# Kernel tuning notes

Measured on AMD Instinct MI355X. Metric: run time of the kernel, lower is better.

## Reference

```python
import jax, jax.numpy as jnp
import numpy as np

N, E, G, D, H, C = 50000, 800000, 64, 128, 4, 32
EPS = 1e-5  # GraphNorm eps


def _gcn(x, W, b, src, dst, n):
    # PyG GCNConv: add self-loops (done by caller), symmetric norm D^-1/2 A D^-1/2
    xw = x @ W
    deg = jax.ops.segment_sum(jnp.ones_like(dst, dtype=xw.dtype), dst, num_segments=n)
    dinv = jnp.where(deg > 0, jax.lax.rsqrt(jnp.maximum(deg, 1e-12)), 0.0)
    norm = dinv[src] * dinv[dst]                      # [E2]
    out = jax.ops.segment_sum(xw[src] * norm[:, None], dst, num_segments=n)
    return out + b


def _gat(x, W, a_src, a_dst, b, src, dst, n):
    # PyG GATConv, heads=H, out C per head, concat, leaky_relu slope 0.2, self-loops added by caller
    h = (x @ W).reshape(n, H, C)
    es = jnp.einsum('nhc,hc->nh', h, a_src)
    ed = jnp.einsum('nhc,hc->nh', h, a_dst)
    e = jax.nn.leaky_relu(es[src] + ed[dst], 0.2)     # [E2,H]
    m = jax.ops.segment_max(e, dst, num_segments=n)   # per-dst softmax (stable)
    e = jnp.exp(e - m[dst])
    s = jax.ops.segment_sum(e, dst, num_segments=n)
    alpha = e / (s[dst] + 1e-16)
    out = jax.ops.segment_sum(h[src] * alpha[:, :, None], dst, num_segments=n)
    return out.reshape(n, H * C) + b


def _graphnorm(x, batch, w, b, ms, g):
    cnt = jnp.maximum(jax.ops.segment_sum(jnp.ones((x.shape[0],), x.dtype), batch, num_segments=g), 1.0)
    mean = jax.ops.segment_sum(x, batch, num_segments=g) / cnt[:, None]
    sub = x - ms * mean[batch]
    var = jax.ops.segment_sum(sub * sub, batch, num_segments=g) / cnt[:, None]
    return w * sub * jax.lax.rsqrt(var[batch] + EPS) + b


def setup_inputs() -> dict:
    key = jax.random.key(0)
    ks = jax.random.split(key, 40)

    def lin(k, din, dout):
        return jax.random.normal(k, (din, dout), jnp.float32) * np.float32((2.0 / (din + dout)) ** 0.5)

    inp = {
        'x': jax.random.normal(ks[0], (N, D), jnp.float32),
        'edge_index': jax.random.randint(ks[1], (2, E), 0, N, dtype=jnp.int32),
        'batch': jnp.sort(jax.random.randint(ks[2], (N,), 0, G, dtype=jnp.int32)),
        'Wp': lin(ks[3], D, D), 'bp': jnp.zeros((D,), jnp.float32),
        'Wg': lin(ks[4], D, D), 'bg': jnp.zeros((D,), jnp.float32),
        'Wa1': lin(ks[5], D, H * C), 'as1': jax.random.normal(ks[6], (H, C), jnp.float32) * 0.1,
        'ad1': jax.random.normal(ks[7], (H, C), jnp.float32) * 0.1, 'ba1': jnp.zeros((D,), jnp.float32),
        'Wa2': lin(ks[8], D, H * C), 'as2': jax.random.normal(ks[9], (H, C), jnp.float32) * 0.1,
        'ad2': jax.random.normal(ks[10], (H, C), jnp.float32) * 0.1, 'ba2': jnp.zeros((D,), jnp.float32),
        'gnw0': jnp.ones((D,), jnp.float32), 'gnb0': jnp.zeros((D,), jnp.float32), 'gns0': jnp.ones((D,), jnp.float32),
        'gnw1': jnp.ones((D,), jnp.float32), 'gnb1': jnp.zeros((D,), jnp.float32), 'gns1': jnp.ones((D,), jnp.float32),
        'gnw2': jnp.ones((D,), jnp.float32), 'gnb2': jnp.zeros((D,), jnp.float32), 'gns2': jnp.ones((D,), jnp.float32),
        'hw1': lin(ks[11], 2 * D, D), 'hb1': jnp.zeros((D,), jnp.float32),
        'hw2': lin(ks[12], D, D // 2), 'hb2': jnp.zeros((D // 2,), jnp.float32),
        'hw3': lin(ks[13], D // 2, 2), 'hb3': jnp.zeros((2,), jnp.float32),
        'nw1': lin(ks[14], D, D // 2), 'nb1': jnp.zeros((D // 2,), jnp.float32),
        'nw2': lin(ks[15], D // 2, 1), 'nb2': jnp.zeros((1,), jnp.float32),
    }
    return inp


def reference(x, edge_index, batch, Wp, bp, Wg, bg, Wa1, as1, ad1, ba1, Wa2, as2, ad2, ba2,
              gnw0, gnb0, gns0, gnw1, gnb1, gns1, gnw2, gnb2, gns2,
              hw1, hb1, hw2, hb2, hw3, hb3, nw1, nb1, nw2, nb2):
    n = x.shape[0]
    loop = jnp.arange(n, dtype=edge_index.dtype)
    src = jnp.concatenate([edge_index[0], loop])
    dst = jnp.concatenate([edge_index[1], loop])

    x = x @ Wp + bp
    h = _graphnorm(_gcn(x, Wg, bg, src, dst, n), batch, gnw0, gnb0, gns0, G)
    x = jax.nn.relu(h) + x  # dropout is identity in eval mode
    h = _graphnorm(_gat(x, Wa1, as1, ad1, ba1, src, dst, n), batch, gnw1, gnb1, gns1, G)
    x = jax.nn.relu(h) + x
    h = _graphnorm(_gat(x, Wa2, as2, ad2, ba2, src, dst, n), batch, gnw2, gnb2, gns2, G)
    x = jax.nn.relu(h) + x

    node_hub_scores = jax.nn.sigmoid((jax.nn.relu(x @ nw1 + nb1) @ nw2 + nb2)[:, 0])

    cnt = jnp.maximum(jax.ops.segment_sum(jnp.ones((n,), x.dtype), batch, num_segments=G), 1.0)
    gmean = jax.ops.segment_sum(x, batch, num_segments=G) / cnt[:, None]
    gmax = jax.ops.segment_max(x, batch, num_segments=G)
    graph_features = jnp.concatenate([gmean, gmax], axis=1)  # [G, 2D]

    z = jax.nn.relu(graph_features @ hw1 + hb1)
    z = jax.nn.relu(z @ hw2 + hb2)
    logits = z @ hw3 + hb3
    return (logits, node_hub_scores, graph_features, x)
```

## Files before the change

### kernel.cpp

```cpp
#include <hip/hip_runtime.h>
#include <cstdint>

#define D 128
#define GG 64
#define SLICES 16
#define NXCD 8

typedef short bf16x8 __attribute__((ext_vector_type(8)));
typedef float f32x4 __attribute__((ext_vector_type(4)));

__device__ inline unsigned short bf16u(float f) {
  unsigned u = __float_as_uint(f);
  u = (u + 0x7FFFu + ((u >> 16) & 1u)) >> 16;
  return (unsigned short)u;
}
__device__ inline float2 unpackbf2(unsigned u) {
  return make_float2(__uint_as_float(u << 16), __uint_as_float(u & 0xFFFF0000u));
}
__device__ inline void accum8(float* acc, uint4 v, float w) {
  float2 p0 = unpackbf2(v.x), p1 = unpackbf2(v.y), p2 = unpackbf2(v.z), p3 = unpackbf2(v.w);
  acc[0] += p0.x * w; acc[1] += p0.y * w; acc[2] += p1.x * w; acc[3] += p1.y * w;
  acc[4] += p2.x * w; acc[5] += p2.y * w; acc[6] += p3.x * w; acc[7] += p3.y * w;
}

__global__ void count_edges_k(const int* __restrict__ dst, int* __restrict__ cnt, int E) {
  int e = blockIdx.x * blockDim.x + threadIdx.x;
  if (e < E) atomicAdd(&cnt[dst[e]], 1);
}

__global__ void bounds_init_k(int* __restrict__ gstart, int* __restrict__ gend) {
  int g = threadIdx.x;
  gstart[g] = 0;
  gend[g] = 0;
}

__global__ void graph_bounds_k(const int* __restrict__ batch, int* __restrict__ gstart,
                               int* __restrict__ gend, int n) {
  int i = blockIdx.x * blockDim.x + threadIdx.x;
  if (i >= n) return;
  int b = batch[i];
  if (i == 0) {
    gstart[b] = 0;
  } else {
    int pb = batch[i - 1];
    if (pb != b) { gstart[b] = i; gend[pb] = i; }
  }
  if (i == n - 1) gend[b] = n;
}

__global__ void gcnt_k(const int* __restrict__ gstart, const int* __restrict__ gend,
                       int* __restrict__ gcnt) {
  int g = threadIdx.x;
  gcnt[g] = gend[g] - gstart[g];
}

__global__ __launch_bounds__(256) void scan1_k(const int* __restrict__ cnt, int* __restrict__ rp,
                                               int* __restrict__ bsum, int n) {
  __shared__ int sd[256];
  int t = threadIdx.x;
  int i = blockIdx.x * 256 + t;
  int v = (i < n) ? cnt[i] : 0;
  sd[t] = v;
  __syncthreads();
#pragma unroll
  for (int off = 1; off < 256; off <<= 1) {
    int u = (t >= off) ? sd[t - off] : 0;
    __syncthreads();
    sd[t] += u;
    __syncthreads();
  }
  if (i < n) rp[i] = sd[t] - v;
  if (t == 255) bsum[blockIdx.x] = sd[255];
}

__global__ __launch_bounds__(256) void scan2_k(int* __restrict__ bsum, int nb) {
  __shared__ int sd[256];
  int t = threadIdx.x;
  int v = (t < nb) ? bsum[t] : 0;
  sd[t] = v;
  __syncthreads();
#pragma unroll
  for (int off = 1; off < 256; off <<= 1) {
    int u = (t >= off) ? sd[t - off] : 0;
    __syncthreads();
    sd[t] += u;
    __syncthreads();
  }
  if (t < nb) bsum[t] = sd[t] - v;
}

__global__ __launch_bounds__(256) void scan3_k(int* __restrict__ rp, const int* __restrict__ bsum,
                                               int* __restrict__ cur, const int* __restrict__ cnt,
                                               float* __restrict__ dinv, int n, int E) {
  int i = blockIdx.x * 256 + threadIdx.x;
  if (i < n) {
    int r = rp[i] + bsum[blockIdx.x];
    rp[i] = r;
    cur[i] = r;
    dinv[i] = rsqrtf((float)cnt[i] + 1.0f);
  }
  if (i == 0) rp[n] = E;
}

__global__ __launch_bounds__(256) void fill_csr_xcd_k(const int* __restrict__ src,
                                                      const int* __restrict__ dst,
                                                      int* __restrict__ cur,
                                                      unsigned short* __restrict__ col,
                                                      int E, int slice) {
  int pass = blockIdx.x & (NXCD - 1);
  int e = (blockIdx.x >> 3) * 256 + threadIdx.x;
  if (e >= E) return;
  int d = dst[e];
  if ((unsigned)(d - pass * slice) < (unsigned)slice) {
    int p = atomicAdd(&cur[d], 1);
    col[p] = (unsigned short)src[e];
  }
}

__global__ void cast_bf16_k(const float* __restrict__ in, unsigned short* __restrict__ outp, int n4) {
  int i = blockIdx.x * blockDim.x + threadIdx.x;
  if (i >= n4) return;
  float4 v = ((const float4*)in)[i];
  ushort4 o;
  o.x = bf16u(v.x); o.y = bf16u(v.y); o.z = bf16u(v.z); o.w = bf16u(v.w);
  ((ushort4*)outp)[i] = o;
}

__global__ void packB_k(const float* __restrict__ B, unsigned short* __restrict__ Bp, int ldb, int ct) {
  int idx = blockIdx.x * 256 + threadIdx.x;
  if (idx >= ct * 256) return;
  int lane = idx & 63;
  int kc = (idx >> 6) & 3;
  int c = idx >> 8;
  int kb = kc * 32 + (lane >> 4) * 8;
  int colq = c * 16 + (lane & 15);
  unsigned short o[8];
#pragma unroll
  for (int j = 0; j < 8; ++j) o[j] = bf16u(B[(size_t)(kb + j) * ldb + colq]);
  uint4 p;
  p.x = (unsigned)o[0] | ((unsigned)o[1] << 16);
  p.y = (unsigned)o[2] | ((unsigned)o[3] << 16);
  p.z = (unsigned)o[4] | ((unsigned)o[5] << 16);
  p.w = (unsigned)o[6] | ((unsigned)o[7] << 16);
  *(uint4*)&Bp[(size_t)idx * 8] = p;
}

__global__ __launch_bounds__(256) void gemm_mfma_k(const unsigned short* __restrict__ Ab,
                                                   const unsigned short* __restrict__ Bp,
                                                   const float* __restrict__ bias,
                                                   float* __restrict__ Cf,
                                                   unsigned short* __restrict__ Cb,
                                                   const float* __restrict__ rowscale,
                                                   const float* __restrict__ as_flat,
                                                   const float* __restrict__ ad_flat,
                                                   float* __restrict__ es, float* __restrict__ ed,
                                                   int M) {
  __shared__ unsigned short Bs[16384];
  int t = threadIdx.x;
  for (int i = t; i < 2048; i += 256) ((uint4*)Bs)[i] = ((const uint4*)Bp)[i];
  __syncthreads();
  int w = t >> 6, lane = t & 63;
  int row0 = blockIdx.x * 64 + w * 16;
  int arow = row0 + (lane & 15);
  f32x4 acc[8];
#pragma unroll
  for (int c = 0; c < 8; ++c) acc[c] = {0.f, 0.f, 0.f, 0.f};
#pragma unroll
  for (int kc = 0; kc < 4; ++kc) {
    bf16x8 a = {0, 0, 0, 0, 0, 0, 0, 0};
    if (arow < M) a = *(const bf16x8*)&Ab[(size_t)arow * 128 + kc * 32 + (lane >> 4) * 8];
#pragma unroll
    for (int c = 0; c < 8; ++c) {
      bf16x8 b = *(const bf16x8*)&Bs[((c * 4 + kc) * 64 + lane) * 8];
      acc[c] = __builtin_amdgcn_mfma_f32_16x16x32_bf16(a, b, acc[c], 0, 0, 0);
    }
  }
  int l15 = lane & 15;
  int rbase = row0 + (lane >> 4) * 4;
#pragma unroll
  for (int c = 0; c < 8; ++c) {
    int colq = c * 16 + l15;
    float bb = bias ? bias[colq] : 0.f;
#pragma unroll
    for (int r = 0; r < 4; ++r) {
      int row = rbase + r;
      if (row < M) {
        float v = acc[c][r] + bb;
        if (Cf) Cf[(size_t)row * 128 + colq] = v;
        if (Cb) {
          float rs = rowscale ? rowscale[row] : 1.f;
          Cb[(size_t)row * 128 + colq] = bf16u(v * rs);
        }
      }
    }
  }
  if (as_flat) {
    float pe[4][4], pd[4][4];
#pragma unroll
    for (int h = 0; h < 4; ++h) {
      float a0 = as_flat[h * 32 + l15], a1 = as_flat[h * 32 + 16 + l15];
      float d0 = ad_flat[h * 32 + l15], d1 = ad_flat[h * 32 + 16 + l15];
#pragma unroll
      for (int r = 0; r < 4; ++r) {
        pe[h][r] = acc[2 * h][r] * a0 + acc[2 * h + 1][r] * a1;
        pd[h][r] = acc[2 * h][r] * d0 + acc[2 * h + 1][r] * d1;
      }
    }
#pragma unroll
    for (int off = 1; off < 16; off <<= 1) {
#pragma unroll
      for (int h = 0; h < 4; ++h)
#pragma unroll
        for (int r = 0; r < 4; ++r) {
          pe[h][r] += __shfl_xor(pe[h][r], off, 64);
          pd[h][r] += __shfl_xor(pd[h][r], off, 64);
        }
    }
    int hh = l15 & 3, rr = l15 >> 2;
    int row = rbase + rr;
    if (row < M) {
      es[row * 4 + hh] = pe[hh][rr];
      ed[row * 4 + hh] = pd[hh][rr];
    }
  }
}

__global__ __launch_bounds__(256) void gcn_gather_k(const uint4* __restrict__ xw16,
                                                    const int* __restrict__ rp,
                                                    const unsigned short* __restrict__ col,
                                                    const float* __restrict__ dinv, const float* __restrict__ bias,
                                                    float* __restrict__ out, int n) {
  int i = blockIdx.x * 4 + (threadIdx.x >> 6);
  if (i >= n) return;
  int lane = threadIdx.x & 63;
  int g = lane >> 4, sub = lane & 15;
  int e0 = __builtin_amdgcn_readfirstlane(rp[i]);
  int e1 = __builtin_amdgcn_readfirstlane(rp[i + 1]);
  float acc[8] = {0.f, 0.f, 0.f, 0.f, 0.f, 0.f, 0.f, 0.f};
  if (g == 0) {
    uint4 v = xw16[(size_t)i * 16 + sub];
    accum8(acc, v, 1.f);
  }
  int e = e0;
  for (; e + 15 < e1; e += 16) {
    int s0 = col[e + g];
    int s1 = col[e + 4 + g];
    int s2 = col[e + 8 + g];
    int s3 = col[e + 12 + g];
    uint4 v0 = xw16[(size_t)s0 * 16 + sub];
    uint4 v1 = xw16[(size_t)s1 * 16 + sub];
    uint4 v2 = xw16[(size_t)s2 * 16 + sub];
    uint4 v3 = xw16[(size_t)s3 * 16 + sub];
    accum8(acc, v0, 1.f); accum8(acc, v1, 1.f); accum8(acc, v2, 1.f); accum8(acc, v3, 1.f);
  }
  for (; e < e1; e += 4) {
    bool ok = (e + g) < e1;
    int s0 = ok ? (int)col[e + g] : i;
    float w0 = ok ? 1.f : 0.f;
    uint4 v0 = xw16[(size_t)s0 * 16 + sub];
    accum8(acc, v0, w0);
  }
#pragma unroll
  for (int k = 0; k < 8; ++k) {
    acc[k] += __shfl_xor(acc[k], 16, 64);
    acc[k] += __shfl_xor(acc[k], 32, 64);
  }
  if (g == 0) {
    float di = dinv[i];
    float4 b0 = ((const float4*)bias)[sub * 2], b1 = ((const float4*)bias)[sub * 2 + 1];
    *(float4*)&out[(size_t)i * 128 + sub * 8] =
        make_float4(acc[0] * di + b0.x, acc[1] * di + b0.y, acc[2] * di + b0.z, acc[3] * di + b0.w);
    *(float4*)&out[(size_t)i * 128 + sub * 8 + 4] =
        make_float4(acc[4] * di + b1.x, acc[5] * di + b1.y, acc[6] * di + b1.z, acc[7] * di + b1.w);
  }
}

__global__ __launch_bounds__(256) void gat_gather_k(const uint4* __restrict__ hf16,
                                                    const int* __restrict__ rp,
                                                    const unsigned short* __restrict__ col,
                                                    const float* __restrict__ es, const float* __restrict__ ed,
                                                    const float* __restrict__ bias, float* __restrict__ out, int n) {
  int i = blockIdx.x * 4 + (threadIdx.x >> 6);
  if (i >= n) return;
  int lane = threadIdx.x & 63;
  int g = lane >> 4, sub = lane & 15;
  int hh = sub >> 2;
  int e0 = __builtin_amdgcn_readfirstlane(rp[i]);
  int e1 = __builtin_amdgcn_readfirstlane(rp[i + 1]);
  float edi = ed[i * 4 + hh];
  float acc[8] = {0.f, 0.f, 0.f, 0.f, 0.f, 0.f, 0.f, 0.f};
  float s = 0.f;
  if (g == 0) {
    float esf = es[i * 4 + hh] + edi;
    esf = esf >= 0.f ? esf : 0.2f * esf;
    float wself = __expf(fminf(esf, 80.f));
    uint4 v = hf16[(size_t)i * 16 + sub];
    accum8(acc, v, wself);
    s = wself;
  }
  int e = e0;
  for (; e + 15 < e1; e += 16) {
    int s0 = col[e + g];
    int s1 = col[e + 4 + g];
    int s2 = col[e + 8 + g];
    int s3 = col[e + 12 + g];
    float t0 = es[s0 * 4 + hh] + edi;
    float t1 = es[s1 * 4 + hh] + edi;
    float t2 = es[s2 * 4 + hh] + edi;
    float t3 = es[s3 * 4 + hh] + edi;
    t0 = t0 >= 0.f ? t0 : 0.2f * t0;
    t1 = t1 >= 0.f ? t1 : 0.2f * t1;
    t2 = t2 >= 0.f ? t2 : 0.2f * t2;
    t3 = t3 >= 0.f ? t3 : 0.2f * t3;
    float w0 = __expf(fminf(t0, 80.f));
    float w1 = __expf(fminf(t1, 80.f));
    float w2 = __expf(fminf(t2, 80.f));
    float w3 = __expf(fminf(t3, 80.f));
    uint4 v0 = hf16[(size_t)s0 * 16 + sub];
    uint4 v1 = hf16[(size_t)s1 * 16 + sub];
    uint4 v2 = hf16[(size_t)s2 * 16 + sub];
    uint4 v3 = hf16[(size_t)s3 * 16 + sub];
    accum8(acc, v0, w0); accum8(acc, v1, w1); accum8(acc, v2, w2); accum8(acc, v3, w3);
    s += w0 + w1 + w2 + w3;
  }
  for (; e < e1; e += 4) {
    bool ok = (e + g) < e1;
    int s0 = ok ? (int)col[e + g] : i;
    float t0 = es[s0 * 4 + hh] + edi;
    t0 = t0 >= 0.f ? t0 : 0.2f * t0;
    float w0 = ok ? __expf(fminf(t0, 80.f)) : 0.f;
    uint4 v0 = hf16[(size_t)s0 * 16 + sub];
    accum8(acc, v0, w0);
    s += w0;
  }
#pragma unroll
  for (int k = 0; k < 8; ++k) {
    acc[k] += __shfl_xor(acc[k], 16, 64);
    acc[k] += __shfl_xor(acc[k], 32, 64);
  }
  s += __shfl_xor(s, 16, 64);
  s += __shfl_xor(s, 32, 64);
  if (g == 0) {
    float wi = 1.0f / s;
    float4 b0 = ((const float4*)bias)[sub * 2], b1 = ((const float4*)bias)[sub * 2 + 1];
    *(float4*)&out[(size_t)i * 128 + sub * 8] =
        make_float4(acc[0] * wi + b0.x, acc[1] * wi + b0.y, acc[2] * wi + b0.z, acc[3] * wi + b0.w);
    *(float4*)&out[(size_t)i * 128 + sub * 8 + 4] =
        make_float4(acc[4] * wi + b1.x, acc[5] * wi + b1.y, acc[6] * wi + b1.z, acc[7] * wi + b1.w);
  }
}

__global__ __launch_bounds__(256) void gn_stats_k(const float* __restrict__ h, const int* __restrict__ gstart,
                                                  const int* __restrict__ gcnt, float* __restrict__ gsum,
                                                  float* __restrict__ gsq) {
  int g = blockIdx.x / SLICES, sl = blockIdx.x % SLICES;
  int st = gstart[g], cn = gcnt[g];
  int d = threadIdx.x & 127, half = threadIdx.x >> 7;
  float s = 0.f, ss = 0.f;
  for (int r = sl * 2 + half; r < cn; r += 2 * SLICES) {
    float v = h[(size_t)(st + r) * D + d];
    s += v; ss += v * v;
  }
  __shared__ float l1[128], l2[128];
  if (half) { l1[d] = s; l2[d] = ss; }
  __syncthreads();
  if (!half) {
    atomicAdd(&gsum[g * D + d], s + l1[d]);
    atomicAdd(&gsq[g * D + d], ss + l2[d]);
  }
}

__global__ void gn_finalize_k(const float* __restrict__ gsum, const float* __restrict__ gsq,
                              const int* __restrict__ gcnt, const float* __restrict__ ms,
                              float* __restrict__ mean, float* __restrict__ rstd) {
  int g = blockIdx.x, d = threadIdx.x;
  float cnt = fmaxf((float)gcnt[g], 1.0f);
  float mu = gsum[g * D + d] / cnt;
  float m2 = gsq[g * D + d] / cnt;
  float s = ms[d];
  float var = m2 - (2.0f * s - s * s) * mu * mu;
  mean[g * D + d] = mu;
  rstd[g * D + d] = rsqrtf(fmaxf(var, 0.0f) + 1e-5f);
}

__global__ void gn_apply_k(const float* __restrict__ h, float* __restrict__ x,
                           unsigned short* __restrict__ xb,
                           const int* __restrict__ batch, const float* __restrict__ mean,
                           const float* __restrict__ rstd, const float* __restrict__ w,
                           const float* __restrict__ b, const float* __restrict__ ms, int n) {
  int idx = blockIdx.x * blockDim.x + threadIdx.x;
  if (idx >= n * 32) return;
  int node = idx >> 5, q = idx & 31;
  int g = batch[node];
  int d0 = q * 4;
  float4 hv = ((const float4*)h)[idx];
  float4 xv = ((const float4*)x)[idx];
  float ha[4] = {hv.x, hv.y, hv.z, hv.w};
  float xa[4] = {xv.x, xv.y, xv.z, xv.w};
  float ra[4];
#pragma unroll
  for (int j = 0; j < 4; ++j) {
    int d = d0 + j;
    float sub = ha[j] - ms[d] * mean[g * D + d];
    float v = w[d] * sub * rstd[g * D + d] + b[d];
    ra[j] = fmaxf(v, 0.f) + xa[j];
  }
  ((float4*)x)[idx] = make_float4(ra[0], ra[1], ra[2], ra[3]);
  ushort4 o;
  o.x = bf16u(ra[0]); o.y = bf16u(ra[1]); o.z = bf16u(ra[2]); o.w = bf16u(ra[3]);
  ((ushort4*)xb)[idx] = o;
}

__global__ __launch_bounds__(256) void hub_mfma_k(const unsigned short* __restrict__ Xb,
                                                  const unsigned short* __restrict__ W1p,
                                                  const float* __restrict__ nb1, const float* __restrict__ nw2,
                                                  const float* __restrict__ nb2, float* __restrict__ out, int n) {
  __shared__ unsigned short Bs[8192];
  int t = threadIdx.x;
  for (int i = t; i < 1024; i += 256) ((uint4*)Bs)[i] = ((const uint4*)W1p)[i];
  __syncthreads();
  int w = t >> 6, lane = t & 63;
  int row0 = blockIdx.x * 64 + w * 16;
  int arow = row0 + (lane & 15);
  f32x4 acc[4];
#pragma unroll
  for (int c = 0; c < 4; ++c) acc[c] = {0.f, 0.f, 0.f, 0.f};
#pragma unroll
  for (int kc = 0; kc < 4; ++kc) {
    bf16x8 a = {0, 0, 0, 0, 0, 0, 0, 0};
    if (arow < n) a = *(const bf16x8*)&Xb[(size_t)arow * 128 + kc * 32 + (lane >> 4) * 8];
#pragma unroll
    for (int c = 0; c < 4; ++c) {
      bf16x8 b = *(const bf16x8*)&Bs[((c * 4 + kc) * 64 + lane) * 8];
      acc[c] = __builtin_amdgcn_mfma_f32_16x16x32_bf16(a, b, acc[c], 0, 0, 0);
    }
  }
  float b2 = nb2[0];
  float s[4] = {0.f, 0.f, 0.f, 0.f};
#pragma unroll
  for (int c = 0; c < 4; ++c) {
    int colq = c * 16 + (lane & 15);
    float b1 = nb1[colq];
    float w2 = nw2[colq];
#pragma unroll
    for (int r = 0; r < 4; ++r) s[r] += fmaxf(acc[c][r] + b1, 0.f) * w2;
  }
#pragma unroll
  for (int off = 1; off < 16; off <<= 1) {
#pragma unroll
    for (int r = 0; r < 4; ++r) s[r] += __shfl_xor(s[r], off, 64);
  }
  if ((lane & 15) == 0) {
    int rbase = row0 + (lane >> 4) * 4;
#pragma unroll
    for (int r = 0; r < 4; ++r) {
      int row = rbase + r;
      if (row < n) out[row] = 1.0f / (1.0f + __expf(-(s[r] + b2)));
    }
  }
}

__global__ void init_maxu_k(unsigned* __restrict__ p, int n) {
  int i = blockIdx.x * blockDim.x + threadIdx.x;
  if (i < n) p[i] = 0x007FFFFFu;
}

__global__ __launch_bounds__(256) void pool_stats_k(const float* __restrict__ x, const int* __restrict__ gstart,
                                                    const int* __restrict__ gcnt, float* __restrict__ gsum,
                                                    unsigned* __restrict__ gmaxu) {
  int g = blockIdx.x / SLICES, sl = blockIdx.x % SLICES;
  int st = gstart[g], cn = gcnt[g];
  int d = threadIdx.x & 127, half = threadIdx.x >> 7;
  float s = 0.f, mx = __uint_as_float(0xFF800000u);
  for (int r = sl * 2 + half; r < cn; r += 2 * SLICES) {
    float v = x[(size_t)(st + r) * D + d];
    s += v; mx = fmaxf(mx, v);
  }
  __shared__ float l1[128], l2[128];
  if (half) { l1[d] = s; l2[d] = mx; }
  __syncthreads();
  if (!half) {
    s += l1[d];
    mx = fmaxf(mx, l2[d]);
    atomicAdd(&gsum[g * D + d], s);
    unsigned u = __float_as_uint(mx);
    u = (u & 0x80000000u) ? ~u : (u | 0x80000000u);
    atomicMax(&gmaxu[g * D + d], u);
  }
}

__global__ void pool_fin_k(const float* __restrict__ gsum, const unsigned* __restrict__ gmaxu,
                           const int* __restrict__ gcnt, float* __restrict__ gf) {
  int g = blockIdx.x, d = threadIdx.x;
  float cnt = fmaxf((float)gcnt[g], 1.0f);
  gf[g * 256 + d] = gsum[g * D + d] / cnt;
  unsigned u = gmaxu[g * D + d];
  unsigned bits = (u & 0x80000000u) ? (u ^ 0x80000000u) : ~u;
  gf[g * 256 + 128 + d] = __uint_as_float(bits);
}

__global__ __launch_bounds__(128) void mlp_k(const float* __restrict__ gf, const float* __restrict__ hw1,
                                             const float* __restrict__ hb1, const float* __restrict__ hw2,
                                             const float* __restrict__ hb2, const float* __restrict__ hw3,
                                             const float* __restrict__ hb3, float* __restrict__ logits) {
  __shared__ float sg[256], z1[128], z2[64];
  int g = blockIdx.x, t = threadIdx.x;
  sg[t] = gf[g * 256 + t];
  sg[t + 128] = gf[g * 256 + 128 + t];
  __syncthreads();
  float a = hb1[t];
  for (int k = 0; k < 256; ++k) a += sg[k] * hw1[k * 128 + t];
  z1[t] = fmaxf(a, 0.f);
  __syncthreads();
  if (t < 64) {
    float a2 = hb2[t];
    for (int k = 0; k < 128; ++k) a2 += z1[k] * hw2[k * 64 + t];
    z2[t] = fmaxf(a2, 0.f);
  }
  __syncthreads();
  if (t < 2) {
    float a3 = hb3[t];
    for (int k = 0; k < 64; ++k) a3 += z2[k] * hw3[k * 2 + t];
    logits[g * 2 + t] = a3;
  }
}

extern "C" void kernel_launch(void* const* d_in, const int* in_sizes, int n_in,
                              void* d_out, int out_size, void* d_ws, size_t ws_size,
                              hipStream_t stream) {
  const float* x_in  = (const float*)d_in[0];
  const int*   eidx  = (const int*)d_in[1];
  const int*   batch = (const int*)d_in[2];
  const float* Wp  = (const float*)d_in[3];
  const float* bp  = (const float*)d_in[4];
  const float* Wg  = (const float*)d_in[5];
  const float* bg  = (const float*)d_in[6];
  const float* Wa1 = (const float*)d_in[7];
  const float* as1 = (const float*)d_in[8];
  const float* ad1 = (const float*)d_in[9];
  const float* ba1 = (const float*)d_in[10];
  const float* Wa2 = (const float*)d_in[11];
  const float* as2 = (const float*)d_in[12];
  const float* ad2 = (const float*)d_in[13];
  const float* ba2 = (const float*)d_in[14];
  const float* gnw[3] = {(const float*)d_in[15], (const float*)d_in[18], (const float*)d_in[21]};
  const float* gnb[3] = {(const float*)d_in[16], (const float*)d_in[19], (const float*)d_in[22]};
  const float* gns[3] = {(const float*)d_in[17], (const float*)d_in[20], (const float*)d_in[23]};
  const float* hw1 = (const float*)d_in[24];
  const float* hb1 = (const float*)d_in[25];
  const float* hw2 = (const float*)d_in[26];
  const float* hb2 = (const float*)d_in[27];
  const float* hw3 = (const float*)d_in[28];
  const float* hb3 = (const float*)d_in[29];
  const float* nw1 = (const float*)d_in[30];
  const float* nb1 = (const float*)d_in[31];
  const float* nw2 = (const float*)d_in[32];
  const float* nb2 = (const float*)d_in[33];

  const int N = in_sizes[0] / D;
  const int E = in_sizes[1] / 2;
  const int* src = eidx;
  const int* dst = eidx + E;

  float* out    = (float*)d_out;
  float* logits = out;
  float* hub    = out + GG * 2;
  float* gf     = out + GG * 2 + N;
  float* X      = out + GG * 2 + N + GG * 256;

  char* wp = (char*)d_ws;
  auto alloc = [&](size_t bytes) { char* p = wp; wp += (bytes + 255) & ~(size_t)255; return p; };
  float*    B2    = (float*)alloc((size_t)N * D * 4);
  unsigned* B1h   = (unsigned*)alloc((size_t)N * (D / 2) * 4);
  unsigned short* Xb = (unsigned short*)alloc((size_t)N * D * 2);
  unsigned short* col = (unsigned short*)alloc((size_t)E * 2);
  int*   cnt     = (int*)alloc((size_t)N * 4);
  int*   rowp    = (int*)alloc((size_t)(N + 1) * 4);
  int*   cur     = (int*)alloc((size_t)N * 4);
  float* dinv    = (float*)alloc((size_t)N * 4);
  float* es      = (float*)alloc((size_t)N * 4 * 4);
  float* ed      = (float*)alloc((size_t)N * 4 * 4);
  float* gsum    = (float*)alloc((size_t)GG * D * 4);
  float* gsq     = (float*)alloc((size_t)GG * D * 4);
  unsigned* gmaxu = (unsigned*)alloc((size_t)GG * D * 4);
  float* mean    = (float*)alloc((size_t)GG * D * 4);
  float* rstd    = (float*)alloc((size_t)GG * D * 4);
  int*   gcnt    = (int*)alloc((size_t)GG * 4);
  int*   gstart  = (int*)alloc((size_t)GG * 4);
  int*   gend    = (int*)alloc((size_t)GG * 4);
  int*   bsum    = (int*)alloc((size_t)256 * 4);
  unsigned short* Wpp  = (unsigned short*)alloc(16384 * 2);
  unsigned short* Wgp  = (unsigned short*)alloc(16384 * 2);
  unsigned short* Wa1p = (unsigned short*)alloc(16384 * 2);
  unsigned short* Wa2p = (unsigned short*)alloc(16384 * 2);
  unsigned short* W1p  = (unsigned short*)alloc(8192 * 2);
  unsigned short* xinb = (unsigned short*)B2;
  if ((size_t)(wp - (char*)d_ws) > ws_size) return;

  const int nb = (N + 255) / 256;

  hipMemsetAsync(cnt, 0, (size_t)N * 4, stream);
  count_edges_k<<<(E + 255) / 256, 256, 0, stream>>>(dst, cnt, E);
  bounds_init_k<<<1, GG, 0, stream>>>(gstart, gend);
  graph_bounds_k<<<nb, 256, 0, stream>>>(batch, gstart, gend, N);
  gcnt_k<<<1, GG, 0, stream>>>(gstart, gend, gcnt);
  scan1_k<<<nb, 256, 0, stream>>>(cnt, rowp, bsum, N);
  scan2_k<<<1, 256, 0, stream>>>(bsum, nb);
  scan3_k<<<nb, 256, 0, stream>>>(rowp, bsum, cur, cnt, dinv, N, E);
  {
    int chunks = (E + 255) / 256;
    int slice = (N + NXCD - 1) / NXCD;
    fill_csr_xcd_k<<<chunks * NXCD, 256, 0, stream>>>(src, dst, cur, col, E, slice);
  }

  packB_k<<<8, 256, 0, stream>>>(Wp, Wpp, 128, 8);
  packB_k<<<8, 256, 0, stream>>>(Wg, Wgp, 128, 8);
  packB_k<<<8, 256, 0, stream>>>(Wa1, Wa1p, 128, 8);
  packB_k<<<8, 256, 0, stream>>>(Wa2, Wa2p, 128, 8);
  packB_k<<<4, 256, 0, stream>>>(nw1, W1p, 64, 4);
  cast_bf16_k<<<(N * 32 + 255) / 256, 256, 0, stream>>>(x_in, xinb, N * 32);

  const int gemmGrid = (N + 63) / 64;
  const int aggGrid  = (N + 3) / 4;

  auto graphnorm = [&](int layer) {
    hipMemsetAsync(gsum, 0, 2 * (size_t)GG * D * 4, stream);
    gn_stats_k<<<GG * SLICES, 256, 0, stream>>>(B2, gstart, gcnt, gsum, gsq);
    gn_finalize_k<<<GG, D, 0, stream>>>(gsum, gsq, gcnt, gns[layer], mean, rstd);
    gn_apply_k<<<(N * 32 + 255) / 256, 256, 0, stream>>>(B2, X, Xb, batch, mean, rstd,
                                                         gnw[layer], gnb[layer], gns[layer], N);
  };

  gemm_mfma_k<<<gemmGrid, 256, 0, stream>>>(xinb, Wpp, bp, X, Xb,
                                            nullptr, nullptr, nullptr, nullptr, nullptr, N);

  gemm_mfma_k<<<gemmGrid, 256, 0, stream>>>(Xb, Wgp, nullptr, nullptr, (unsigned short*)B1h,
                                            dinv, nullptr, nullptr, nullptr, nullptr, N);
  gcn_gather_k<<<aggGrid, 256, 0, stream>>>((const uint4*)B1h, rowp, col, dinv, bg, B2, N);
  graphnorm(0);

  gemm_mfma_k<<<gemmGrid, 256, 0, stream>>>(Xb, Wa1p, nullptr, nullptr, (unsigned short*)B1h,
                                            nullptr, as1, ad1, es, ed, N);
  gat_gather_k<<<aggGrid, 256, 0, stream>>>((const uint4*)B1h, rowp, col, es, ed, ba1, B2, N);
  graphnorm(1);

  gemm_mfma_k<<<gemmGrid, 256, 0, stream>>>(Xb, Wa2p, nullptr, nullptr, (unsigned short*)B1h,
                                            nullptr, as2, ad2, es, ed, N);
  gat_gather_k<<<aggGrid, 256, 0, stream>>>((const uint4*)B1h, rowp, col, es, ed, ba2, B2, N);
  graphnorm(2);

  hub_mfma_k<<<gemmGrid, 256, 0, stream>>>(Xb, W1p, nb1, nw2, nb2, hub, N);

  hipMemsetAsync(gsum, 0, (size_t)GG * D * 4, stream);
  init_maxu_k<<<(GG * D + 255) / 256, 256, 0, stream>>>(gmaxu, GG * D);
  pool_stats_k<<<GG * SLICES, 256, 0, stream>>>(X, gstart, gcnt, gsum, gmaxu);
  pool_fin_k<<<GG, D, 0, stream>>>(gsum, gmaxu, gcnt, gf);
  mlp_k<<<GG, 128, 0, stream>>>(gf, hw1, hb1, hw2, hb2, hw3, hb3, logits);
}
```

Before: 414.5 us.

## Store conv outputs in bf16 and compute GAT edge weights once per edge

The GCN and GAT gather kernels now write their pre-norm outputs as packed bf16 instead of fp32, and the GraphNorm stats and apply kernels read bf16. This halves the traffic of that intermediate buffer. The GAT gather computes each edge's attention weight once per lane (one edge per sub-lane, one head per group) and distributes the weights with shuffles, replacing the per-head redundant es loads and exps. Both gathers merge the remainder loop into the main 16-wide loop with predication. The extra bf16 rounding of the pre-norm activations lowers precision.

```diff
diff --git a/kernel.cpp b/kernel.cpp
--- a/kernel.cpp
+++ b/kernel.cpp
@@ -14,6 +14,10 @@
   u = (u + 0x7FFFu + ((u >> 16) & 1u)) >> 16;
   return (unsigned short)u;
 }
+__device__ inline unsigned packbf2(float a, float b) {
+  return (unsigned)bf16u(a) | ((unsigned)bf16u(b) << 16);
+}
+__device__ inline float bfu(unsigned short u) { return __uint_as_float((unsigned)u << 16); }
 __device__ inline float2 unpackbf2(unsigned u) {
   return make_float2(__uint_as_float(u << 16), __uint_as_float(u & 0xFFFF0000u));
 }
@@ -229,7 +233,7 @@
                                                     const int* __restrict__ rp,
                                                     const unsigned short* __restrict__ col,
                                                     const float* __restrict__ dinv, const float* __restrict__ bias,
-                                                    float* __restrict__ out, int n) {
+                                                    unsigned short* __restrict__ outb, int n) {
   int i = blockIdx.x * 4 + (threadIdx.x >> 6);
   if (i >= n) return;
   int lane = threadIdx.x & 63;
@@ -241,24 +245,21 @@
     uint4 v = xw16[(size_t)i * 16 + sub];
     accum8(acc, v, 1.f);
   }
-  int e = e0;
-  for (; e + 15 < e1; e += 16) {
-    int s0 = col[e + g];
-    int s1 = col[e + 4 + g];
-    int s2 = col[e + 8 + g];
-    int s3 = col[e + 12 + g];
+  for (int e = e0; e < e1; e += 16) {
+    int i0 = e + g, i1 = e + 4 + g, i2 = e + 8 + g, i3 = e + 12 + g;
+    int s0 = i0 < e1 ? (int)col[i0] : i;
+    int s1 = i1 < e1 ? (int)col[i1] : i;
+    int s2 = i2 < e1 ? (int)col[i2] : i;
+    int s3 = i3 < e1 ? (int)col[i3] : i;
+    float w0 = i0 < e1 ? 1.f : 0.f;
+    float w1 = i1 < e1 ? 1.f : 0.f;
+    float w2 = i2 < e1 ? 1.f : 0.f;
+    float w3 = i3 < e1 ? 1.f : 0.f;
     uint4 v0 = xw16[(size_t)s0 * 16 + sub];
     uint4 v1 = xw16[(size_t)s1 * 16 + sub];
     uint4 v2 = xw16[(size_t)s2 * 16 + sub];
     uint4 v3 = xw16[(size_t)s3 * 16 + sub];
-    accum8(acc, v0, 1.f); accum8(acc, v1, 1.f); accum8(acc, v2, 1.f); accum8(acc, v3, 1.f);
-  }
-  for (; e < e1; e += 4) {
-    bool ok = (e + g) < e1;
-    int s0 = ok ? (int)col[e + g] : i;
-    float w0 = ok ? 1.f : 0.f;
-    uint4 v0 = xw16[(size_t)s0 * 16 + sub];
-    accum8(acc, v0, w0);
+    accum8(acc, v0, w0); accum8(acc, v1, w1); accum8(acc, v2, w2); accum8(acc, v3, w3);
   }
 #pragma unroll
   for (int k = 0; k < 8; ++k) {
@@ -268,10 +269,12 @@
   if (g == 0) {
     float di = dinv[i];
     float4 b0 = ((const float4*)bias)[sub * 2], b1 = ((const float4*)bias)[sub * 2 + 1];
-    *(float4*)&out[(size_t)i * 128 + sub * 8] =
-        make_float4(acc[0] * di + b0.x, acc[1] * di + b0.y, acc[2] * di + b0.z, acc[3] * di + b0.w);
-    *(float4*)&out[(size_t)i * 128 + sub * 8 + 4] =
-        make_float4(acc[4] * di + b1.x, acc[5] * di + b1.y, acc[6] * di + b1.z, acc[7] * di + b1.w);
+    uint4 p;
+    p.x = packbf2(acc[0] * di + b0.x, acc[1] * di + b0.y);
+    p.y = packbf2(acc[2] * di + b0.z, acc[3] * di + b0.w);
+    p.z = packbf2(acc[4] * di + b1.x, acc[5] * di + b1.y);
+    p.w = packbf2(acc[6] * di + b1.z, acc[7] * di + b1.w);
+    ((uint4*)outb)[(size_t)i * 16 + sub] = p;
   }
 }
 
@@ -279,7 +282,8 @@
                                                     const int* __restrict__ rp,
                                                     const unsigned short* __restrict__ col,
                                                     const float* __restrict__ es, const float* __restrict__ ed,
-                                                    const float* __restrict__ bias, float* __restrict__ out, int n) {
+                                                    const float* __restrict__ bias,
+                                                    unsigned short* __restrict__ outb, int n) {
   int i = blockIdx.x * 4 + (threadIdx.x >> 6);
   if (i >= n) return;
   int lane = threadIdx.x & 63;
@@ -287,35 +291,34 @@
   int hh = sub >> 2;
   int e0 = __builtin_amdgcn_readfirstlane(rp[i]);
   int e1 = __builtin_amdgcn_readfirstlane(rp[i + 1]);
-  float edi = ed[i * 4 + hh];
+  float edi_g = ed[i * 4 + g];
   float acc[8] = {0.f, 0.f, 0.f, 0.f, 0.f, 0.f, 0.f, 0.f};
   float s = 0.f;
   if (g == 0) {
-    float esf = es[i * 4 + hh] + edi;
+    float esf = es[i * 4 + hh] + ed[i * 4 + hh];
     esf = esf >= 0.f ? esf : 0.2f * esf;
     float wself = __expf(fminf(esf, 80.f));
     uint4 v = hf16[(size_t)i * 16 + sub];
     accum8(acc, v, wself);
     s = wself;
   }
-  int e = e0;
-  for (; e + 15 < e1; e += 16) {
-    int s0 = col[e + g];
-    int s1 = col[e + 4 + g];
-    int s2 = col[e + 8 + g];
-    int s3 = col[e + 12 + g];
-    float t0 = es[s0 * 4 + hh] + edi;
-    float t1 = es[s1 * 4 + hh] + edi;
-    float t2 = es[s2 * 4 + hh] + edi;
-    float t3 = es[s3 * 4 + hh] + edi;
-    t0 = t0 >= 0.f ? t0 : 0.2f * t0;
-    t1 = t1 >= 0.f ? t1 : 0.2f * t1;
-    t2 = t2 >= 0.f ? t2 : 0.2f * t2;
-    t3 = t3 >= 0.f ? t3 : 0.2f * t3;
-    float w0 = __expf(fminf(t0, 80.f));
-    float w1 = __expf(fminf(t1, 80.f));
-    float w2 = __expf(fminf(t2, 80.f));
-    float w3 = __expf(fminf(t3, 80.f));
+  for (int e = e0; e < e1; e += 16) {
+    int el = e + sub;
+    bool okl = el < e1;
+    int sl = okl ? (int)col[el] : i;
+    float tl = es[sl * 4 + g] + edi_g;
+    tl = tl >= 0.f ? tl : 0.2f * tl;
+    float wl = okl ? __expf(fminf(tl, 80.f)) : 0.f;
+    int base = hh << 4;
+    float w0 = __shfl(wl, base | g, 64);
+    float w1 = __shfl(wl, base | (g + 4), 64);
+    float w2 = __shfl(wl, base | (g + 8), 64);
+    float w3 = __shfl(wl, base | (g + 12), 64);
+    int i0 = e + g, i1 = e + 4 + g, i2 = e + 8 + g, i3 = e + 12 + g;
+    int s0 = i0 < e1 ? (int)col[i0] : i;
+    int s1 = i1 < e1 ? (int)col[i1] : i;
+    int s2 = i2 < e1 ? (int)col[i2] : i;
+    int s3 = i3 < e1 ? (int)col[i3] : i;
     uint4 v0 = hf16[(size_t)s0 * 16 + sub];
     uint4 v1 = hf16[(size_t)s1 * 16 + sub];
     uint4 v2 = hf16[(size_t)s2 * 16 + sub];
@@ -323,16 +326,6 @@
     accum8(acc, v0, w0); accum8(acc, v1, w1); accum8(acc, v2, w2); accum8(acc, v3, w3);
     s += w0 + w1 + w2 + w3;
   }
-  for (; e < e1; e += 4) {
-    bool ok = (e + g) < e1;
-    int s0 = ok ? (int)col[e + g] : i;
-    float t0 = es[s0 * 4 + hh] + edi;
-    t0 = t0 >= 0.f ? t0 : 0.2f * t0;
-    float w0 = ok ? __expf(fminf(t0, 80.f)) : 0.f;
-    uint4 v0 = hf16[(size_t)s0 * 16 + sub];
-    accum8(acc, v0, w0);
-    s += w0;
-  }
 #pragma unroll
   for (int k = 0; k < 8; ++k) {
     acc[k] += __shfl_xor(acc[k], 16, 64);
@@ -343,14 +336,17 @@
   if (g == 0) {
     float wi = 1.0f / s;
     float4 b0 = ((const float4*)bias)[sub * 2], b1 = ((const float4*)bias)[sub * 2 + 1];
-    *(float4*)&out[(size_t)i * 128 + sub * 8] =
-        make_float4(acc[0] * wi + b0.x, acc[1] * wi + b0.y, acc[2] * wi + b0.z, acc[3] * wi + b0.w);
-    *(float4*)&out[(size_t)i * 128 + sub * 8 + 4] =
-        make_float4(acc[4] * wi + b1.x, acc[5] * wi + b1.y, acc[6] * wi + b1.z, acc[7] * wi + b1.w);
-  }
-}
-
-__global__ __launch_bounds__(256) void gn_stats_k(const float* __restrict__ h, const int* __restrict__ gstart,
+    uint4 p;
+    p.x = packbf2(acc[0] * wi + b0.x, acc[1] * wi + b0.y);
+    p.y = packbf2(acc[2] * wi + b0.z, acc[3] * wi + b0.w);
+    p.z = packbf2(acc[4] * wi + b1.x, acc[5] * wi + b1.y);
+    p.w = packbf2(acc[6] * wi + b1.z, acc[7] * wi + b1.w);
+    ((uint4*)outb)[(size_t)i * 16 + sub] = p;
+  }
+}
+
+__global__ __launch_bounds__(256) void gn_stats_k(const unsigned short* __restrict__ h,
+                                                  const int* __restrict__ gstart,
                                                   const int* __restrict__ gcnt, float* __restrict__ gsum,
                                                   float* __restrict__ gsq) {
   int g = blockIdx.x / SLICES, sl = blockIdx.x % SLICES;
@@ -358,7 +354,7 @@
   int d = threadIdx.x & 127, half = threadIdx.x >> 7;
   float s = 0.f, ss = 0.f;
   for (int r = sl * 2 + half; r < cn; r += 2 * SLICES) {
-    float v = h[(size_t)(st + r) * D + d];
+    float v = bfu(h[(size_t)(st + r) * D + d]);
     s += v; ss += v * v;
   }
   __shared__ float l1[128], l2[128];
@@ -383,7 +379,7 @@
   rstd[g * D + d] = rsqrtf(fmaxf(var, 0.0f) + 1e-5f);
 }
 
-__global__ void gn_apply_k(const float* __restrict__ h, float* __restrict__ x,
+__global__ void gn_apply_k(const unsigned short* __restrict__ h, float* __restrict__ x,
                            unsigned short* __restrict__ xb,
                            const int* __restrict__ batch, const float* __restrict__ mean,
                            const float* __restrict__ rstd, const float* __restrict__ w,
@@ -393,9 +389,9 @@
   int node = idx >> 5, q = idx & 31;
   int g = batch[node];
   int d0 = q * 4;
-  float4 hv = ((const float4*)h)[idx];
+  ushort4 hv = ((const ushort4*)h)[idx];
   float4 xv = ((const float4*)x)[idx];
-  float ha[4] = {hv.x, hv.y, hv.z, hv.w};
+  float ha[4] = {bfu(hv.x), bfu(hv.y), bfu(hv.z), bfu(hv.w)};
   float xa[4] = {xv.x, xv.y, xv.z, xv.w};
   float ra[4];
 #pragma unroll
@@ -570,7 +566,7 @@
 
   char* wp = (char*)d_ws;
   auto alloc = [&](size_t bytes) { char* p = wp; wp += (bytes + 255) & ~(size_t)255; return p; };
-  float*    B2    = (float*)alloc((size_t)N * D * 4);
+  unsigned short* B2 = (unsigned short*)alloc((size_t)N * D * 2);
   unsigned* B1h   = (unsigned*)alloc((size_t)N * (D / 2) * 4);
   unsigned short* Xb = (unsigned short*)alloc((size_t)N * D * 2);
   unsigned short* col = (unsigned short*)alloc((size_t)E * 2);
@@ -594,7 +590,7 @@
   unsigned short* Wa1p = (unsigned short*)alloc(16384 * 2);
   unsigned short* Wa2p = (unsigned short*)alloc(16384 * 2);
   unsigned short* W1p  = (unsigned short*)alloc(8192 * 2);
-  unsigned short* xinb = (unsigned short*)B2;
+  unsigned short* xinb = B2;
   if ((size_t)(wp - (char*)d_ws) > ws_size) return;
 
   const int nb = (N + 255) / 256;
```

After: 404.6 us. 2.4% less time.
